# Performance work log

Measured on AMD Instinct MI355X. Metric: run time of the kernel, lower is better.

## Reference

```python
import jax, jax.numpy as jnp
import numpy as np

N_NODES = 50000
N_EDGES = 800000
N_GRAPHS = 64
EPS = 1e-12


def setup_inputs() -> dict:
    key = jax.random.key(0)
    ks = jax.random.split(key, 8)
    x = jax.random.normal(ks[0], (N_NODES, 128), dtype=jnp.float32)
    edge_index = jax.random.randint(ks[1], (2, N_EDGES), 0, N_NODES, dtype=jnp.int64)
    batch = jnp.sort(jax.random.randint(ks[2], (N_NODES,), 0, N_GRAPHS, dtype=jnp.int64))
    W1 = jax.random.normal(ks[3], (128, 64), dtype=jnp.float32) * 0.1
    W2 = jax.random.normal(ks[4], (64, 64), dtype=jnp.float32) * 0.1
    W3 = jax.random.normal(ks[5], (64, 64), dtype=jnp.float32) * 0.1
    Wl = jax.random.normal(ks[6], (128, 32), dtype=jnp.float32) * 0.1
    return {
        'x': x, 'edge_index': edge_index, 'batch': batch,
        'W1': W1, 'b1': jnp.zeros((64,), jnp.float32),
        'W2': W2, 'b2': jnp.zeros((64,), jnp.float32),
        'W3': W3, 'b3': jnpp if False else jnp.zeros((64,), jnp.float32),
        'Wl': Wl, 'bl': jnp.zeros((32,), jnp.float32),
    }


def _gcn_conv(h, W, b, src, dst, dinv, enorm, n):
    # PyG GCNConv: D^-1/2 (A+I) D^-1/2 (h W) + b, self-loops included analytically
    hw = h @ W
    agg = jax.ops.segment_sum(hw[src] * enorm[:, None], dst, num_segments=n)
    agg = agg + (dinv * dinv)[:, None] * hw  # self-loop term
    return agg + b


def _norm_relu(h):
    # F.normalize(p=2, dim=1) then relu
    nrm = jnp.sqrt(jnp.sum(h * h, axis=1, keepdims=True))
    return jax.nn.relu(h / jnp.maximum(nrm, EPS))


def reference(x, edge_index, batch, W1, b1, W2, b2, W3, b3, Wl, bl):
    n = x.shape[0]
    src, dst = edge_index[0], edge_index[1]
    # degree with self-loops (counts incoming edges at target, +1 for self-loop)
    deg = jax.ops.segment_sum(jnp.ones((src.shape[0],), x.dtype), dst, num_segments=n) + 1.0
    dinv = 1.0 / jnp.sqrt(deg)
    enorm = dinv[src] * dinv[dst]

    h = _norm_relu(_gcn_conv(x, W1, b1, src, dst, dinv, enorm, n))
    h = _norm_relu(_gcn_conv(h, W2, b2, src, dst, dinv, enorm, n))
    h = _norm_relu(_gcn_conv(h, W3, b3, src, dst, dinv, enorm, n))

    counts = jax.ops.segment_sum(jnp.ones((n,), x.dtype), batch, num_segments=N_GRAPHS)
    x_mean = jax.ops.segment_sum(h, batch, num_segments=N_GRAPHS) / jnp.maximum(counts, 1.0)[:, None]
    x_max = jax.ops.segment_max(h, batch, num_segments=N_GRAPHS)
    x_max = jnp.where(counts[:, None] > 0, x_max, 0.0)  # guard empty graphs

    pooled = jnp.concatenate([x_mean, x_max], axis=-1)  # [B, 2*hidden]
    return pooled @ Wl + bl
```

## Files before the change

kernel.cpp:

```cpp
#include <hip/hip_runtime.h>
#include <hip/hip_bf16.h>

#define N_NODES 50000
#define N_EDGES 800000
#define N_GRAPHS 64
#define HID 64
#define SCAN_NB 196
#define FILL_RANGES 8
#define RANGE_SIZE ((N_NODES + FILL_RANGES - 1) / FILL_RANGES)

static inline size_t align256(size_t x) { return (x + 255) & ~(size_t)255; }

typedef __attribute__((ext_vector_type(8))) short short8v;
typedef __attribute__((ext_vector_type(4))) float f32x4;

__device__ __forceinline__ unsigned short f2bf(float f) {
    unsigned int u = __float_as_uint(f);
    unsigned int r = (u + 0x7fffu + ((u >> 16) & 1u)) >> 16;
    return (unsigned short)r;
}
__device__ __forceinline__ float bf2f(unsigned short h) {
    return __uint_as_float(((unsigned int)h) << 16);
}

__global__ void zero_i32(int* __restrict__ p, int n) {
    int i = blockIdx.x * blockDim.x + threadIdx.x;
    if (i < n) p[i] = 0;
}

__global__ void deg_kernel(const int* __restrict__ ei, int* __restrict__ cnt) {
    int e = blockIdx.x * blockDim.x + threadIdx.x;
    if (e < N_EDGES) atomicAdd(&cnt[ei[N_EDGES + e]], 1);
}

__global__ __launch_bounds__(256) void scan_a(const int* __restrict__ cnt,
                                              int* __restrict__ incl,
                                              int* __restrict__ bsum) {
    __shared__ int sd[256];
    int t = threadIdx.x;
    int i = blockIdx.x * 256 + t;
    int v = (i < N_NODES) ? cnt[i] : 0;
    sd[t] = v;
    __syncthreads();
    for (int off = 1; off < 256; off <<= 1) {
        int u = (t >= off) ? sd[t - off] : 0;
        __syncthreads();
        sd[t] += u;
        __syncthreads();
    }
    if (i < N_NODES) incl[i] = sd[t];
    if (t == 255) bsum[blockIdx.x] = sd[255];
}

__global__ __launch_bounds__(256) void scan_b(const int* __restrict__ bsum,
                                              int* __restrict__ boff) {
    __shared__ int sd[256];
    int t = threadIdx.x;
    int v = (t < SCAN_NB) ? bsum[t] : 0;
    sd[t] = v;
    __syncthreads();
    for (int off = 1; off < 256; off <<= 1) {
        int u = (t >= off) ? sd[t - off] : 0;
        __syncthreads();
        sd[t] += u;
        __syncthreads();
    }
    if (t < SCAN_NB) boff[t] = sd[t] - v;
}

__global__ void scan_c(const int* __restrict__ cnt, const int* __restrict__ incl,
                       const int* __restrict__ boff, int* __restrict__ row_ptr,
                       int* __restrict__ fill_ptr, float* __restrict__ dinv) {
    int i = blockIdx.x * blockDim.x + threadIdx.x;
    if (i < N_NODES) {
        int c = cnt[i];
        int run = boff[i >> 8] + incl[i];
        row_ptr[i + 1] = run;
        fill_ptr[i] = run - c;
        dinv[i] = rsqrtf((float)c + 1.0f);
        if (i == 0) row_ptr[0] = 0;
    }
}

__global__ __launch_bounds__(256) void fill_kernel(const int* __restrict__ ei,
                                                   int* __restrict__ fill_ptr,
                                                   int* __restrict__ csr_src) {
    int r = blockIdx.x & (FILL_RANGES - 1);
    int e = (blockIdx.x >> 3) * 256 + threadIdx.x;
    if (e >= N_EDGES) return;
    int dst = ei[N_EDGES + e];
    int lo = r * RANGE_SIZE;
    if (dst >= lo && dst < lo + RANGE_SIZE) {
        int src = ei[e];
        int pos = atomicAdd(&fill_ptr[dst], 1);
        csr_src[pos] = src;
    }
}

__global__ void gstart_kernel(const int* __restrict__ batch, int* __restrict__ gstart) {
    int g = threadIdx.x;
    if (g <= N_GRAPHS) {
        int lo = 0, hi = N_NODES;
        while (lo < hi) {
            int mid = (lo + hi) >> 1;
            if (batch[mid] < g) lo = mid + 1; else hi = mid;
        }
        gstart[g] = lo;
    }
}

template <int K>
__global__ __launch_bounds__(256) void mfma_matmul(const float* __restrict__ h,
                                                   const float* __restrict__ W,
                                                   const float* __restrict__ dinv,
                                                   unsigned short* __restrict__ hw2) {
    constexpr int NSTEP = K / 32;
    __shared__ unsigned short sWH[NSTEP * 4 * 64 * 8];
    __shared__ unsigned short sWL[NSTEP * 4 * 64 * 8];
    int tid = threadIdx.x;
    int r0 = blockIdx.x * 64;

#pragma unroll 1
    for (int ent = tid; ent < NSTEP * 4 * 64; ent += 256) {
        int lane_e = ent & 63;
        int c = (ent >> 6) & 3;
        int step = ent >> 8;
        int kb = step * 32 + (lane_e >> 4) * 8;
        int n = c * 16 + (lane_e & 15);
#pragma unroll
        for (int j = 0; j < 8; ++j) {
            float f = W[(kb + j) * 64 + n];
            unsigned short hi = f2bf(f);
            sWH[ent * 8 + j] = hi;
            sWL[ent * 8 + j] = f2bf(f - bf2f(hi));
        }
    }
    __syncthreads();

    int lane = tid & 63;
    int wid = tid >> 6;
    int arow = min(r0 + wid * 16 + (lane & 15), N_NODES - 1);
    const float* ap = h + (size_t)arow * K;
    int klane = (lane >> 4) * 8;

    f32x4 acc[4];
#pragma unroll
    for (int c = 0; c < 4; ++c) acc[c] = (f32x4){0.f, 0.f, 0.f, 0.f};

#pragma unroll 1
    for (int step = 0; step < NSTEP; ++step) {
        int kb = step * 32 + klane;
        float4 f0 = *(const float4*)&ap[kb];
        float4 f1 = *(const float4*)&ap[kb + 4];
        float fv[8] = {f0.x, f0.y, f0.z, f0.w, f1.x, f1.y, f1.z, f1.w};
        short8v ahi, alo;
#pragma unroll
        for (int j = 0; j < 8; ++j) {
            unsigned short hi = f2bf(fv[j]);
            ahi[j] = (short)hi;
            alo[j] = (short)f2bf(fv[j] - bf2f(hi));
        }
#pragma unroll
        for (int c = 0; c < 4; ++c) {
            short8v bh = *(const short8v*)&sWH[((step * 4 + c) * 64 + lane) * 8];
            short8v bl = *(const short8v*)&sWL[((step * 4 + c) * 64 + lane) * 8];
            acc[c] = __builtin_amdgcn_mfma_f32_16x16x32_bf16(ahi, bh, acc[c], 0, 0, 0);
            acc[c] = __builtin_amdgcn_mfma_f32_16x16x32_bf16(alo, bh, acc[c], 0, 0, 0);
            acc[c] = __builtin_amdgcn_mfma_f32_16x16x32_bf16(ahi, bl, acc[c], 0, 0, 0);
        }
    }

    int rb = r0 + wid * 16 + (lane >> 4) * 4;
#pragma unroll
    for (int j = 0; j < 4; ++j) {
        int row = rb + j;
        if (row < N_NODES) {
            float dv = dinv[row];
#pragma unroll
            for (int c = 0; c < 4; ++c) {
                hw2[(size_t)row * 64 + c * 16 + (lane & 15)] = f2bf(dv * acc[c][j]);
            }
        }
    }
}

__global__ __launch_bounds__(256) void agg_kernel(const unsigned short* __restrict__ hw2,
                                                  const int* __restrict__ row_ptr,
                                                  const int* __restrict__ csr_src,
                                                  const float* __restrict__ dinv,
                                                  const float* __restrict__ b,
                                                  float* __restrict__ hout) {
    int node = blockIdx.x * 4 + (threadIdx.x >> 6);
    int lane = threadIdx.x & 63;
    if (node >= N_NODES) return;
    int grp = lane >> 4;
    int gl  = lane & 15;
    int s = row_ptr[node], e = row_ptr[node + 1];

    float ax = 0.f, ay = 0.f, az = 0.f, aw = 0.f;
    for (int base = s; base < e; base += 64) {
        int nE = min(64, e - base);
        int msrc = (lane < nE) ? csr_src[base + lane] : 0;
#pragma unroll 2
        for (int i = 0; i < nE; i += 4) {
            int myi = i + grp;
            int src = __shfl(msrc, myi, 64);
            if (myi < nE) {
                ushort4 v = *(const ushort4*)&hw2[(size_t)src * 64 + gl * 4];
                ax += bf2f(v.x); ay += bf2f(v.y); az += bf2f(v.z); aw += bf2f(v.w);
            }
        }
    }
#pragma unroll
    for (int off = 16; off <= 32; off <<= 1) {
        ax += __shfl_xor(ax, off, 64);
        ay += __shfl_xor(ay, off, 64);
        az += __shfl_xor(az, off, 64);
        aw += __shfl_xor(aw, off, 64);
    }
    ushort4 sv = *(const ushort4*)&hw2[(size_t)node * 64 + gl * 4];
    ax += bf2f(sv.x); ay += bf2f(sv.y); az += bf2f(sv.z); aw += bf2f(sv.w);

    float di = dinv[node];
    float4 bb = *(const float4*)&b[gl * 4];
    float vx = di * ax + bb.x;
    float vy = di * ay + bb.y;
    float vz = di * az + bb.z;
    float vw = di * aw + bb.w;

    float sq = vx * vx + vy * vy + vz * vz + vw * vw;
#pragma unroll
    for (int off = 1; off <= 8; off <<= 1) sq += __shfl_xor(sq, off, 64);
    float inv = 1.0f / fmaxf(sqrtf(sq), 1e-12f);

    if (grp == 0) {
        float4 r;
        r.x = fmaxf(vx * inv, 0.f);
        r.y = fmaxf(vy * inv, 0.f);
        r.z = fmaxf(vz * inv, 0.f);
        r.w = fmaxf(vw * inv, 0.f);
        *(float4*)&hout[(size_t)node * 64 + gl * 4] = r;
    }
}

__global__ __launch_bounds__(256) void pool_partial_kernel(const float* __restrict__ h,
                                                           const int* __restrict__ batch,
                                                           float* __restrict__ gsum,
                                                           float* __restrict__ gmax) {
    int wid = threadIdx.x >> 6, lane = threadIdx.x & 63;
    int i0 = blockIdx.x * 64 + wid * 16;
    if (i0 >= N_NODES) return;
    int i1 = min(i0 + 16, N_NODES);
    int gcur = batch[i0];
    float sum = 0.f, mx = 0.f;
    for (int i = i0; i < i1; ++i) {
        int g = batch[i];
        if (g != gcur) {
            atomicAdd(&gsum[gcur * 64 + lane], sum);
            atomicMax((int*)&gmax[gcur * 64 + lane], __float_as_int(mx));
            sum = 0.f; mx = 0.f; gcur = g;
        }
        float v = h[(size_t)i * 64 + lane];
        sum += v;
        mx = fmaxf(mx, v);
    }
    atomicAdd(&gsum[gcur * 64 + lane], sum);
    atomicMax((int*)&gmax[gcur * 64 + lane], __float_as_int(mx));
}

__global__ __launch_bounds__(128) void linear_kernel(const float* __restrict__ gsum,
                                                     const float* __restrict__ gmax,
                                                     const int* __restrict__ gstart,
                                                     const float* __restrict__ Wl,
                                                     const float* __restrict__ bl,
                                                     float* __restrict__ out) {
    int g = blockIdx.x;
    __shared__ float pooled[128];
    int t = threadIdx.x;
    if (t < 64) {
        int cnt = gstart[g + 1] - gstart[g];
        pooled[t] = gsum[g * 64 + t] / fmaxf((float)cnt, 1.0f);
    } else {
        pooled[t] = gmax[g * 64 + (t - 64)];
    }
    __syncthreads();
    if (t < 32) {
        float acc = bl[t];
#pragma unroll 8
        for (int k = 0; k < 128; ++k) acc += pooled[k] * Wl[k * 32 + t];
        out[g * 32 + t] = acc;
    }
}

extern "C" void kernel_launch(void* const* d_in, const int* in_sizes, int n_in,
                              void* d_out, int out_size, void* d_ws, size_t ws_size,
                              hipStream_t stream) {
    const float* x        = (const float*)d_in[0];
    const int*   ei       = (const int*)d_in[1];
    const int*   batch    = (const int*)d_in[2];
    const float* W1       = (const float*)d_in[3];
    const float* b1       = (const float*)d_in[4];
    const float* W2       = (const float*)d_in[5];
    const float* b2       = (const float*)d_in[6];
    const float* W3       = (const float*)d_in[7];
    const float* b3       = (const float*)d_in[8];
    const float* Wl       = (const float*)d_in[9];
    const float* bl       = (const float*)d_in[10];
    float* out = (float*)d_out;

    char* ws = (char*)d_ws;
    int*   cnt      = (int*)ws;                 ws += align256((size_t)N_NODES * 4);
    int*   incl     = (int*)ws;                 ws += align256((size_t)N_NODES * 4);
    int*   bsum     = (int*)ws;                 ws += align256((size_t)SCAN_NB * 4);
    int*   boff     = (int*)ws;                 ws += align256((size_t)SCAN_NB * 4);
    int*   row_ptr  = (int*)ws;                 ws += align256((size_t)(N_NODES + 1) * 4);
    int*   fill_ptr = (int*)ws;                 ws += align256((size_t)N_NODES * 4);
    float* dinv     = (float*)ws;               ws += align256((size_t)N_NODES * 4);
    int*   gstart   = (int*)ws;                 ws += align256((size_t)(N_GRAPHS + 1) * 4);
    float* gsum     = (float*)ws;               ws += align256((size_t)N_GRAPHS * 64 * 4);
    float* gmax     = (float*)ws;               ws += align256((size_t)N_GRAPHS * 64 * 4);
    int*   csr_src  = (int*)ws;                 ws += align256((size_t)N_EDGES * 4);
    unsigned short* hwb = (unsigned short*)ws;  ws += align256((size_t)N_NODES * 64 * 2);
    float* h1       = (float*)ws;               ws += align256((size_t)N_NODES * 64 * 4);
    float* h2       = (float*)ws;               ws += align256((size_t)N_NODES * 64 * 4);

    hipLaunchKernelGGL(zero_i32, dim3((N_NODES + 255) / 256), dim3(256), 0, stream, cnt, N_NODES);
    hipLaunchKernelGGL(zero_i32, dim3((2 * N_GRAPHS * 64 + 255) / 256), dim3(256), 0, stream,
                       (int*)gsum, 2 * N_GRAPHS * 64);
    hipLaunchKernelGGL(deg_kernel, dim3((N_EDGES + 255) / 256), dim3(256), 0, stream, ei, cnt);
    hipLaunchKernelGGL(scan_a, dim3(SCAN_NB), dim3(256), 0, stream, cnt, incl, bsum);
    hipLaunchKernelGGL(scan_b, dim3(1), dim3(256), 0, stream, bsum, boff);
    hipLaunchKernelGGL(scan_c, dim3(SCAN_NB), dim3(256), 0, stream,
                       cnt, incl, boff, row_ptr, fill_ptr, dinv);
    hipLaunchKernelGGL(fill_kernel,
                       dim3(FILL_RANGES * ((N_EDGES + 255) / 256)), dim3(256), 0, stream,
                       ei, fill_ptr, csr_src);
    hipLaunchKernelGGL(gstart_kernel, dim3(1), dim3(128), 0, stream, batch, gstart);

    const int mm_grid = (N_NODES + 63) / 64;
    const int agg_grid = (N_NODES + 3) / 4;

    hipLaunchKernelGGL((mfma_matmul<128>), dim3(mm_grid), dim3(256), 0, stream, x, W1, dinv, hwb);
    hipLaunchKernelGGL(agg_kernel, dim3(agg_grid), dim3(256), 0, stream,
                       hwb, row_ptr, csr_src, dinv, b1, h1);
    hipLaunchKernelGGL((mfma_matmul<64>), dim3(mm_grid), dim3(256), 0, stream, h1, W2, dinv, hwb);
    hipLaunchKernelGGL(agg_kernel, dim3(agg_grid), dim3(256), 0, stream,
                       hwb, row_ptr, csr_src, dinv, b2, h2);
    hipLaunchKernelGGL((mfma_matmul<64>), dim3(mm_grid), dim3(256), 0, stream, h2, W3, dinv, hwb);
    hipLaunchKernelGGL(agg_kernel, dim3(agg_grid), dim3(256), 0, stream,
                       hwb, row_ptr, csr_src, dinv, b3, h1);

    hipLaunchKernelGGL(pool_partial_kernel, dim3((N_NODES + 63) / 64), dim3(256), 0, stream,
                       h1, batch, gsum, gmax);
    hipLaunchKernelGGL(linear_kernel, dim3(N_GRAPHS), dim3(128), 0, stream,
                       gsum, gmax, gstart, Wl, bl, out);
}
```

Before: 223.6 us.

## Fuse aggregation with next-layer matmul and merge small setup kernels

Adds an aggregation kernel that also applies normalize+relu and multiplies by the next layer's weight matrix from shared memory, then writes the bf16 pre-scaled features directly. This removes the fp32 intermediate write and read and two separate MFMA matmul launches for layers 2 and 3. Setup is also consolidated: the two zeroing kernels merge into one, and the graph-start search folds into the single-block scan kernel. In exchange, the matmul runs in fp32 on scalar ALUs through wave shuffles instead of MFMA, and every block reloads the 16KB weight tile into shared memory.

```diff
diff --git a/kernel.cpp b/kernel.cpp
--- a/kernel.cpp
+++ b/kernel.cpp
@@ -23,9 +23,10 @@
     return __uint_as_float(((unsigned int)h) << 16);
 }
 
-__global__ void zero_i32(int* __restrict__ p, int n) {
+__global__ void zero2(int* __restrict__ a, int na, int* __restrict__ b, int nb) {
     int i = blockIdx.x * blockDim.x + threadIdx.x;
-    if (i < n) p[i] = 0;
+    if (i < na) a[i] = 0;
+    else if (i < na + nb) b[i - na] = 0;
 }
 
 __global__ void deg_kernel(const int* __restrict__ ei, int* __restrict__ cnt) {
@@ -52,20 +53,34 @@
     if (t == 255) bsum[blockIdx.x] = sd[255];
 }
 
-__global__ __launch_bounds__(256) void scan_b(const int* __restrict__ bsum,
-                                              int* __restrict__ boff) {
+__global__ __launch_bounds__(384) void scan_b_gstart(const int* __restrict__ bsum,
+                                                     int* __restrict__ boff,
+                                                     const int* __restrict__ batch,
+                                                     int* __restrict__ gstart) {
     __shared__ int sd[256];
     int t = threadIdx.x;
-    int v = (t < SCAN_NB) ? bsum[t] : 0;
-    sd[t] = v;
+    int v = 0;
+    if (t < 256) {
+        v = (t < SCAN_NB) ? bsum[t] : 0;
+        sd[t] = v;
+    }
     __syncthreads();
     for (int off = 1; off < 256; off <<= 1) {
-        int u = (t >= off) ? sd[t - off] : 0;
+        int u = (t < 256 && t >= off) ? sd[t - off] : 0;
         __syncthreads();
-        sd[t] += u;
+        if (t < 256) sd[t] += u;
         __syncthreads();
     }
     if (t < SCAN_NB) boff[t] = sd[t] - v;
+    if (t >= 256 && t - 256 <= N_GRAPHS) {
+        int g = t - 256;
+        int lo = 0, hi = N_NODES;
+        while (lo < hi) {
+            int mid = (lo + hi) >> 1;
+            if (batch[mid] < g) lo = mid + 1; else hi = mid;
+        }
+        gstart[g] = lo;
+    }
 }
 
 __global__ void scan_c(const int* __restrict__ cnt, const int* __restrict__ incl,
@@ -97,18 +112,6 @@
     }
 }
 
-__global__ void gstart_kernel(const int* __restrict__ batch, int* __restrict__ gstart) {
-    int g = threadIdx.x;
-    if (g <= N_GRAPHS) {
-        int lo = 0, hi = N_NODES;
-        while (lo < hi) {
-            int mid = (lo + hi) >> 1;
-            if (batch[mid] < g) lo = mid + 1; else hi = mid;
-        }
-        gstart[g] = lo;
-    }
-}
-
 template <int K>
 __global__ __launch_bounds__(256) void mfma_matmul(const float* __restrict__ h,
                                                    const float* __restrict__ W,
@@ -182,6 +185,83 @@
             }
         }
     }
+}
+
+__global__ __launch_bounds__(256) void aggmm_kernel(const unsigned short* __restrict__ hw_in,
+                                                    const int* __restrict__ row_ptr,
+                                                    const int* __restrict__ csr_src,
+                                                    const float* __restrict__ dinv,
+                                                    const float* __restrict__ b,
+                                                    const float* __restrict__ Wn,
+                                                    unsigned short* __restrict__ hw_out) {
+    __shared__ float sW[64 * 64];
+    int tid = threadIdx.x;
+#pragma unroll 1
+    for (int i = tid * 4; i < 64 * 64; i += 256 * 4)
+        *(float4*)&sW[i] = *(const float4*)&Wn[i];
+    __syncthreads();
+
+    int node = blockIdx.x * 4 + (tid >> 6);
+    int lane = tid & 63;
+    if (node >= N_NODES) return;
+    int grp = lane >> 4;
+    int gl  = lane & 15;
+    int s = row_ptr[node], e = row_ptr[node + 1];
+
+    float ax = 0.f, ay = 0.f, az = 0.f, aw = 0.f;
+    for (int base = s; base < e; base += 64) {
+        int nE = min(64, e - base);
+        int msrc = (lane < nE) ? csr_src[base + lane] : 0;
+#pragma unroll 2
+        for (int i = 0; i < nE; i += 4) {
+            int myi = i + grp;
+            int src = __shfl(msrc, myi, 64);
+            if (myi < nE) {
+                ushort4 v = *(const ushort4*)&hw_in[(size_t)src * 64 + gl * 4];
+                ax += bf2f(v.x); ay += bf2f(v.y); az += bf2f(v.z); aw += bf2f(v.w);
+            }
+        }
+    }
+#pragma unroll
+    for (int off = 16; off <= 32; off <<= 1) {
+        ax += __shfl_xor(ax, off, 64);
+        ay += __shfl_xor(ay, off, 64);
+        az += __shfl_xor(az, off, 64);
+        aw += __shfl_xor(aw, off, 64);
+    }
+    ushort4 sv = *(const ushort4*)&hw_in[(size_t)node * 64 + gl * 4];
+    ax += bf2f(sv.x); ay += bf2f(sv.y); az += bf2f(sv.z); aw += bf2f(sv.w);
+
+    float di = dinv[node];
+    float4 bb = *(const float4*)&b[gl * 4];
+    float vx = di * ax + bb.x;
+    float vy = di * ay + bb.y;
+    float vz = di * az + bb.z;
+    float vw = di * aw + bb.w;
+
+    float sq = vx * vx + vy * vy + vz * vz + vw * vw;
+#pragma unroll
+    for (int off = 1; off <= 8; off <<= 1) sq += __shfl_xor(sq, off, 64);
+    float inv = 1.0f / fmaxf(sqrtf(sq), 1e-12f);
+
+    float rx = fmaxf(vx * inv, 0.f);
+    float ry = fmaxf(vy * inv, 0.f);
+    float rz = fmaxf(vz * inv, 0.f);
+    float rw = fmaxf(vw * inv, 0.f);
+
+    float acc = 0.f;
+#pragma unroll
+    for (int q = 0; q < 16; ++q) {
+        float h0 = __shfl(rx, q, 64);
+        float h1 = __shfl(ry, q, 64);
+        float h2 = __shfl(rz, q, 64);
+        float h3 = __shfl(rw, q, 64);
+        acc += h0 * sW[(4 * q + 0) * 64 + lane];
+        acc += h1 * sW[(4 * q + 1) * 64 + lane];
+        acc += h2 * sW[(4 * q + 2) * 64 + lane];
+        acc += h3 * sW[(4 * q + 3) * 64 + lane];
+    }
+    hw_out[(size_t)node * 64 + lane] = f2bf(di * acc);
 }
 
 __global__ __launch_bounds__(256) void agg_kernel(const unsigned short* __restrict__ hw2,
@@ -320,35 +400,31 @@
     float* gsum     = (float*)ws;               ws += align256((size_t)N_GRAPHS * 64 * 4);
     float* gmax     = (float*)ws;               ws += align256((size_t)N_GRAPHS * 64 * 4);
     int*   csr_src  = (int*)ws;                 ws += align256((size_t)N_EDGES * 4);
-    unsigned short* hwb = (unsigned short*)ws;  ws += align256((size_t)N_NODES * 64 * 2);
+    unsigned short* hwa = (unsigned short*)ws;  ws += align256((size_t)N_NODES * 64 * 2);
+    unsigned short* hwbuf = (unsigned short*)ws; ws += align256((size_t)N_NODES * 64 * 2);
     float* h1       = (float*)ws;               ws += align256((size_t)N_NODES * 64 * 4);
-    float* h2       = (float*)ws;               ws += align256((size_t)N_NODES * 64 * 4);
-
-    hipLaunchKernelGGL(zero_i32, dim3((N_NODES + 255) / 256), dim3(256), 0, stream, cnt, N_NODES);
-    hipLaunchKernelGGL(zero_i32, dim3((2 * N_GRAPHS * 64 + 255) / 256), dim3(256), 0, stream,
-                       (int*)gsum, 2 * N_GRAPHS * 64);
+
+    hipLaunchKernelGGL(zero2, dim3((N_NODES + 2 * N_GRAPHS * 64 + 255) / 256), dim3(256), 0,
+                       stream, cnt, N_NODES, (int*)gsum, 2 * N_GRAPHS * 64);
     hipLaunchKernelGGL(deg_kernel, dim3((N_EDGES + 255) / 256), dim3(256), 0, stream, ei, cnt);
     hipLaunchKernelGGL(scan_a, dim3(SCAN_NB), dim3(256), 0, stream, cnt, incl, bsum);
-    hipLaunchKernelGGL(scan_b, dim3(1), dim3(256), 0, stream, bsum, boff);
+    hipLaunchKernelGGL(scan_b_gstart, dim3(1), dim3(384), 0, stream, bsum, boff, batch, gstart);
     hipLaunchKernelGGL(scan_c, dim3(SCAN_NB), dim3(256), 0, stream,
                        cnt, incl, boff, row_ptr, fill_ptr, dinv);
     hipLaunchKernelGGL(fill_kernel,
                        dim3(FILL_RANGES * ((N_EDGES + 255) / 256)), dim3(256), 0, stream,
                        ei, fill_ptr, csr_src);
-    hipLaunchKernelGGL(gstart_kernel, dim3(1), dim3(128), 0, stream, batch, gstart);
 
     const int mm_grid = (N_NODES + 63) / 64;
     const int agg_grid = (N_NODES + 3) / 4;
 
-    hipLaunchKernelGGL((mfma_matmul<128>), dim3(mm_grid), dim3(256), 0, stream, x, W1, dinv, hwb);
+    hipLaunchKernelGGL((mfma_matmul<128>), dim3(mm_grid), dim3(256), 0, stream, x, W1, dinv, hwa);
+    hipLaunchKernelGGL(aggmm_kernel, dim3(agg_grid), dim3(256), 0, stream,
+                       hwa, row_ptr, csr_src, dinv, b1, W2, hwbuf);
+    hipLaunchKernelGGL(aggmm_kernel, dim3(agg_grid), dim3(256), 0, stream,
+                       hwbuf, row_ptr, csr_src, dinv, b2, W3, hwa);
     hipLaunchKernelGGL(agg_kernel, dim3(agg_grid), dim3(256), 0, stream,
-                       hwb, row_ptr, csr_src, dinv, b1, h1);
-    hipLaunchKernelGGL((mfma_matmul<64>), dim3(mm_grid), dim3(256), 0, stream, h1, W2, dinv, hwb);
-    hipLaunchKernelGGL(agg_kernel, dim3(agg_grid), dim3(256), 0, stream,
-                       hwb, row_ptr, csr_src, dinv, b2, h2);
-    hipLaunchKernelGGL((mfma_matmul<64>), dim3(mm_grid), dim3(256), 0, stream, h2, W3, dinv, hwb);
-    hipLaunchKernelGGL(agg_kernel, dim3(agg_grid), dim3(256), 0, stream,
-                       hwb, row_ptr, csr_src, dinv, b3, h1);
+                       hwa, row_ptr, csr_src, dinv, b3, h1);
 
     hipLaunchKernelGGL(pool_partial_kernel, dim3((N_NODES + 63) / 64), dim3(256), 0, stream,
                        h1, batch, gsum, gmax);
```

New measurement: 269.9 us. 1.21x slower.

## Widen aggregation gathers to 16-byte loads and merge small setup kernels

Applied to the files above, without the earlier changes.

The aggregation kernel now has each lane load 8 bf16 values (16 bytes) per neighbor row, so 8 lanes cover a row and 8 edges are processed per wave iteration instead of 4. The reduction trees are adjusted to match. Separately, the two zeroing kernels are merged into one, and the graph-start binary search is folded into the single-block scan kernel, removing two launches. The wider loads raise per-lane register use and add a longer cross-group shuffle reduction in exchange for fewer, larger memory transactions.

```diff
diff --git a/kernel.cpp b/kernel.cpp
--- a/kernel.cpp
+++ b/kernel.cpp
@@ -23,9 +23,10 @@
     return __uint_as_float(((unsigned int)h) << 16);
 }
 
-__global__ void zero_i32(int* __restrict__ p, int n) {
+__global__ void zero2(int* __restrict__ a, int na, int* __restrict__ b, int nb) {
     int i = blockIdx.x * blockDim.x + threadIdx.x;
-    if (i < n) p[i] = 0;
+    if (i < na) a[i] = 0;
+    else if (i < na + nb) b[i - na] = 0;
 }
 
 __global__ void deg_kernel(const int* __restrict__ ei, int* __restrict__ cnt) {
@@ -52,20 +53,34 @@
     if (t == 255) bsum[blockIdx.x] = sd[255];
 }
 
-__global__ __launch_bounds__(256) void scan_b(const int* __restrict__ bsum,
-                                              int* __restrict__ boff) {
+__global__ __launch_bounds__(384) void scan_b_gstart(const int* __restrict__ bsum,
+                                                     int* __restrict__ boff,
+                                                     const int* __restrict__ batch,
+                                                     int* __restrict__ gstart) {
     __shared__ int sd[256];
     int t = threadIdx.x;
-    int v = (t < SCAN_NB) ? bsum[t] : 0;
-    sd[t] = v;
+    int v = 0;
+    if (t < 256) {
+        v = (t < SCAN_NB) ? bsum[t] : 0;
+        sd[t] = v;
+    }
     __syncthreads();
     for (int off = 1; off < 256; off <<= 1) {
-        int u = (t >= off) ? sd[t - off] : 0;
+        int u = (t < 256 && t >= off) ? sd[t - off] : 0;
         __syncthreads();
-        sd[t] += u;
+        if (t < 256) sd[t] += u;
         __syncthreads();
     }
     if (t < SCAN_NB) boff[t] = sd[t] - v;
+    if (t >= 256 && t - 256 <= N_GRAPHS) {
+        int g = t - 256;
+        int lo = 0, hi = N_NODES;
+        while (lo < hi) {
+            int mid = (lo + hi) >> 1;
+            if (batch[mid] < g) lo = mid + 1; else hi = mid;
+        }
+        gstart[g] = lo;
+    }
 }
 
 __global__ void scan_c(const int* __restrict__ cnt, const int* __restrict__ incl,
@@ -97,18 +112,6 @@
     }
 }
 
-__global__ void gstart_kernel(const int* __restrict__ batch, int* __restrict__ gstart) {
-    int g = threadIdx.x;
-    if (g <= N_GRAPHS) {
-        int lo = 0, hi = N_NODES;
-        while (lo < hi) {
-            int mid = (lo + hi) >> 1;
-            if (batch[mid] < g) lo = mid + 1; else hi = mid;
-        }
-        gstart[g] = lo;
-    }
-}
-
 template <int K>
 __global__ __launch_bounds__(256) void mfma_matmul(const float* __restrict__ h,
                                                    const float* __restrict__ W,
@@ -193,53 +196,66 @@
     int node = blockIdx.x * 4 + (threadIdx.x >> 6);
     int lane = threadIdx.x & 63;
     if (node >= N_NODES) return;
-    int grp = lane >> 4;
-    int gl  = lane & 15;
+    int grp = lane >> 3;
+    int gl  = lane & 7;
     int s = row_ptr[node], e = row_ptr[node + 1];
 
-    float ax = 0.f, ay = 0.f, az = 0.f, aw = 0.f;
+    float acc[8] = {0.f, 0.f, 0.f, 0.f, 0.f, 0.f, 0.f, 0.f};
     for (int base = s; base < e; base += 64) {
         int nE = min(64, e - base);
         int msrc = (lane < nE) ? csr_src[base + lane] : 0;
 #pragma unroll 2
-        for (int i = 0; i < nE; i += 4) {
+        for (int i = 0; i < nE; i += 8) {
             int myi = i + grp;
             int src = __shfl(msrc, myi, 64);
             if (myi < nE) {
-                ushort4 v = *(const ushort4*)&hw2[(size_t)src * 64 + gl * 4];
-                ax += bf2f(v.x); ay += bf2f(v.y); az += bf2f(v.z); aw += bf2f(v.w);
+                short8v v = *(const short8v*)&hw2[(size_t)src * 64 + gl * 8];
+#pragma unroll
+                for (int j = 0; j < 8; ++j) acc[j] += bf2f((unsigned short)v[j]);
             }
         }
     }
 #pragma unroll
-    for (int off = 16; off <= 32; off <<= 1) {
-        ax += __shfl_xor(ax, off, 64);
-        ay += __shfl_xor(ay, off, 64);
-        az += __shfl_xor(az, off, 64);
-        aw += __shfl_xor(aw, off, 64);
-    }
-    ushort4 sv = *(const ushort4*)&hw2[(size_t)node * 64 + gl * 4];
-    ax += bf2f(sv.x); ay += bf2f(sv.y); az += bf2f(sv.z); aw += bf2f(sv.w);
+    for (int off = 8; off <= 32; off <<= 1) {
+#pragma unroll
+        for (int j = 0; j < 8; ++j) acc[j] += __shfl_xor(acc[j], off, 64);
+    }
+    short8v sv = *(const short8v*)&hw2[(size_t)node * 64 + gl * 8];
+#pragma unroll
+    for (int j = 0; j < 8; ++j) acc[j] += bf2f((unsigned short)sv[j]);
 
     float di = dinv[node];
-    float4 bb = *(const float4*)&b[gl * 4];
-    float vx = di * ax + bb.x;
-    float vy = di * ay + bb.y;
-    float vz = di * az + bb.z;
-    float vw = di * aw + bb.w;
-
-    float sq = vx * vx + vy * vy + vz * vz + vw * vw;
-#pragma unroll
-    for (int off = 1; off <= 8; off <<= 1) sq += __shfl_xor(sq, off, 64);
+    float4 b0 = *(const float4*)&b[gl * 8];
+    float4 b1 = *(const float4*)&b[gl * 8 + 4];
+    float val[8];
+    val[0] = di * acc[0] + b0.x;
+    val[1] = di * acc[1] + b0.y;
+    val[2] = di * acc[2] + b0.z;
+    val[3] = di * acc[3] + b0.w;
+    val[4] = di * acc[4] + b1.x;
+    val[5] = di * acc[5] + b1.y;
+    val[6] = di * acc[6] + b1.z;
+    val[7] = di * acc[7] + b1.w;
+
+    float sq = 0.f;
+#pragma unroll
+    for (int j = 0; j < 8; ++j) sq += val[j] * val[j];
+#pragma unroll
+    for (int off = 1; off <= 4; off <<= 1) sq += __shfl_xor(sq, off, 64);
     float inv = 1.0f / fmaxf(sqrtf(sq), 1e-12f);
 
     if (grp == 0) {
-        float4 r;
-        r.x = fmaxf(vx * inv, 0.f);
-        r.y = fmaxf(vy * inv, 0.f);
-        r.z = fmaxf(vz * inv, 0.f);
-        r.w = fmaxf(vw * inv, 0.f);
-        *(float4*)&hout[(size_t)node * 64 + gl * 4] = r;
+        float4 r0, r1;
+        r0.x = fmaxf(val[0] * inv, 0.f);
+        r0.y = fmaxf(val[1] * inv, 0.f);
+        r0.z = fmaxf(val[2] * inv, 0.f);
+        r0.w = fmaxf(val[3] * inv, 0.f);
+        r1.x = fmaxf(val[4] * inv, 0.f);
+        r1.y = fmaxf(val[5] * inv, 0.f);
+        r1.z = fmaxf(val[6] * inv, 0.f);
+        r1.w = fmaxf(val[7] * inv, 0.f);
+        *(float4*)&hout[(size_t)node * 64 + gl * 8] = r0;
+        *(float4*)&hout[(size_t)node * 64 + gl * 8 + 4] = r1;
     }
 }
 
@@ -324,18 +340,16 @@
     float* h1       = (float*)ws;               ws += align256((size_t)N_NODES * 64 * 4);
     float* h2       = (float*)ws;               ws += align256((size_t)N_NODES * 64 * 4);
 
-    hipLaunchKernelGGL(zero_i32, dim3((N_NODES + 255) / 256), dim3(256), 0, stream, cnt, N_NODES);
-    hipLaunchKernelGGL(zero_i32, dim3((2 * N_GRAPHS * 64 + 255) / 256), dim3(256), 0, stream,
-                       (int*)gsum, 2 * N_GRAPHS * 64);
+    hipLaunchKernelGGL(zero2, dim3((N_NODES + 2 * N_GRAPHS * 64 + 255) / 256), dim3(256), 0,
+                       stream, cnt, N_NODES, (int*)gsum, 2 * N_GRAPHS * 64);
     hipLaunchKernelGGL(deg_kernel, dim3((N_EDGES + 255) / 256), dim3(256), 0, stream, ei, cnt);
     hipLaunchKernelGGL(scan_a, dim3(SCAN_NB), dim3(256), 0, stream, cnt, incl, bsum);
-    hipLaunchKernelGGL(scan_b, dim3(1), dim3(256), 0, stream, bsum, boff);
+    hipLaunchKernelGGL(scan_b_gstart, dim3(1), dim3(384), 0, stream, bsum, boff, batch, gstart);
     hipLaunchKernelGGL(scan_c, dim3(SCAN_NB), dim3(256), 0, stream,
                        cnt, incl, boff, row_ptr, fill_ptr, dinv);
     hipLaunchKernelGGL(fill_kernel,
                        dim3(FILL_RANGES * ((N_EDGES + 255) / 256)), dim3(256), 0, stream,
                        ei, fill_ptr, csr_src);
-    hipLaunchKernelGGL(gstart_kernel, dim3(1), dim3(128), 0, stream, batch, gstart);
 
     const int mm_grid = (N_NODES + 63) / 64;
     const int agg_grid = (N_NODES + 3) / 4;
```

After: 212.4 us. 1.05x faster.
